# Performance work log

Measured on AMD Instinct MI355X. Metric: run time of the kernel, lower is better.

Reference implementation:

```python
import jax, jax.numpy as jnp
import numpy as np
import math

D_MODEL = 1024
NUM_HEADS = 16
DIM_FF = 4096
B, N = 4, 1024
GRID = 32
R_LEFT = 1.0
R_RIGHT = 1.0
LN_EPS = 1e-5


def get_alibi_slopes(n_heads):
    def pow2(n):
        start = 2 ** (-2 ** (-(math.log2(n) - 3)))
        return [start * start ** i for i in range(n)]
    if math.log2(n_heads).is_integer():
        slopes = pow2(n_heads)
    else:
        m = 2 ** math.floor(math.log2(n_heads))
        slopes = pow2(m)
        slopes += [slopes[-1] * 0.5 ** (i + 1) for i in range(n_heads - m)]
    return jnp.asarray(np.array(slopes, dtype=np.float32))


def setup_inputs() -> dict:
    key = jax.random.key(0)
    ks = jax.random.split(key, 16)
    s = 1.0 / math.sqrt(D_MODEL)
    inp = {
        "src": jax.random.normal(ks[0], (B, N, D_MODEL), jnp.float32),
        "coords": jax.random.randint(ks[1], (B, N, 2), 0, GRID, jnp.int32),
        "Wq": jax.random.normal(ks[2], (D_MODEL, D_MODEL), jnp.float32) * s,
        "Wk": jax.random.normal(ks[3], (D_MODEL, D_MODEL), jnp.float32) * s,
        "Wv": jax.random.normal(ks[4], (D_MODEL, D_MODEL), jnp.float32) * s,
        "Wo": jax.random.normal(ks[5], (D_MODEL, D_MODEL), jnp.float32) * s,
        "W1": jax.random.normal(ks[6], (DIM_FF, D_MODEL), jnp.float32) * s,
        "b1": jnp.zeros((DIM_FF,), jnp.float32),
        "W2": jax.random.normal(ks[7], (D_MODEL, DIM_FF), jnp.float32) * (1.0 / math.sqrt(DIM_FF)),
        "b2": jnp.zeros((D_MODEL,), jnp.float32),
        "g1": jnp.ones((D_MODEL,), jnp.float32),
        "be1": jnp.zeros((D_MODEL,), jnp.float32),
        "g2": jnp.ones((D_MODEL,), jnp.float32),
        "be2": jnp.zeros((D_MODEL,), jnp.float32),
    }
    return inp


def layer_norm(x, g, b):
    mu = jnp.mean(x, axis=-1, keepdims=True)
    var = jnp.mean(jnp.square(x - mu), axis=-1, keepdims=True)
    return (x - mu) * jax.lax.rsqrt(var + LN_EPS) * g + b


def alibi_2d_bias(coords, slopes):
    # coords: (B, N, 2) int -> bias (B, H, N, N)
    x = coords[..., 0].astype(jnp.float32)
    y = coords[..., 1].astype(jnp.float32)
    dist = jnp.abs(x[:, :, None] - x[:, None, :]) + jnp.abs(y[:, :, None] - y[:, None, :])
    flat = y * (x.max() + 1.0) + x  # global x.max(), matching torch code
    le = (flat[:, None, :] <= flat[:, :, None]).astype(jnp.float32)  # (B,N,N)
    s = slopes.reshape(1, -1, 1, 1)
    left = s * R_LEFT
    right = s * R_RIGHT
    return dist[:, None] * (le[:, None] * left + (1.0 - le[:, None]) * right)


def reference(src, coords, Wq, Wk, Wv, Wo, W1, b1, W2, b2, g1, be1, g2, be2):
    H, Hd = NUM_HEADS, D_MODEL // NUM_HEADS
    scale = Hd ** (-0.5)
    slopes = get_alibi_slopes(H)
    bias = alibi_2d_bias(coords, slopes)  # (B,H,N,N)

    Bn, Nn, D = src.shape
    q = (src @ Wq.T).reshape(Bn, Nn, H, Hd)
    k = (src @ Wk.T).reshape(Bn, Nn, H, Hd)
    v = (src @ Wv.T).reshape(Bn, Nn, H, Hd)
    attn = jnp.einsum("bnhd,bmhd->bhnm", q, k) * scale + bias
    attn = jax.nn.softmax(attn, axis=-1)
    out = jnp.einsum("bhnm,bmhd->bnhd", attn, v).reshape(Bn, Nn, D)
    src2 = out @ Wo.T

    x = layer_norm(src + src2, g1, be1)
    ff = (jax.nn.gelu(x @ W1.T + b1, approximate=False)) @ W2.T + b2
    return layer_norm(x + ff, g2, be2)
```

## Files before the change

### kernel.cpp

```cpp
#include <hip/hip_runtime.h>
#include <hip/hip_bf16.h>
#include <math.h>

#define DEV __device__ __forceinline__

typedef __attribute__((ext_vector_type(4))) float f32x4;
typedef __attribute__((ext_vector_type(16))) float f32x16;
typedef __attribute__((ext_vector_type(8))) short bf16x8;
typedef __attribute__((ext_vector_type(4))) unsigned short us4;

DEV unsigned short f2bf(float f) {
    union { float f; unsigned u; } v; v.f = f;
    unsigned r = v.u + 0x7FFF + ((v.u >> 16) & 1);
    return (unsigned short)(r >> 16);
}

DEV void async16(const void* g, void* l) {
    __builtin_amdgcn_global_load_lds(
        (const __attribute__((address_space(1))) void*)g,
        (__attribute__((address_space(3))) void*)l, 16, 0, 0);
}

DEV int xcd_swizzle(int flat, int nwg) {
    int q = nwg >> 3, r8 = nwg & 7;
    int xcd = flat & 7, idx = flat >> 3;
    return (xcd < r8 ? xcd * (q + 1) : r8 * (q + 1) + (xcd - r8) * q) + idx;
}

__global__ void cvt_kernel(const float* __restrict__ in, unsigned short* __restrict__ out, int n4) {
    int i = blockIdx.x * blockDim.x + threadIdx.x;
    if (i >= n4) return;
    f32x4 v = ((const f32x4*)in)[i];
    us4 o;
    o.x = f2bf(v.x); o.y = f2bf(v.y); o.z = f2bf(v.z); o.w = f2bf(v.w);
    ((us4*)out)[i] = o;
}

#define BM 128
#define BN 128
#define BKK 64

template<int EPI>
__global__ __launch_bounds__(256) void gemm_bt(
    const unsigned short* __restrict__ A,
    const unsigned short* __restrict__ B,
    float* __restrict__ Cf, unsigned short* __restrict__ Cb,
    const float* __restrict__ bias,
    int M, int N, int K)
{
    __shared__ unsigned short As[BM * BKK];
    __shared__ unsigned short Bs[BN * BKK];

    const int tid  = threadIdx.x;
    const int wid  = tid >> 6, lane = tid & 63;
    const int l15  = lane & 15, l16 = lane >> 4;
    const int wr   = wid >> 1, wc = wid & 1;

    const int nwg  = gridDim.x * gridDim.y;
    const int flat = xcd_swizzle(blockIdx.y * gridDim.x + blockIdx.x, nwg);
    const int row0 = (flat / gridDim.x) * BM;
    const int col0 = (flat % gridDim.x) * BN;

    f32x4 acc[4][4] = {};

    const int nkt = K / BKK;
    for (int kt = 0; kt < nkt; ++kt) {
        const int k0 = kt * BKK;
        __syncthreads();
#pragma unroll
        for (int i = 0; i < 4; ++i) {
            int c = i * 256 + tid;
            int row = c >> 3, slot = c & 7;
            int ks = (slot ^ (row & 7)) * 8;
            async16(A + (size_t)(row0 + row) * K + k0 + ks, (char*)As + c * 16);
            async16(B + (size_t)(col0 + row) * K + k0 + ks, (char*)Bs + c * 16);
        }
        __syncthreads();
#pragma unroll
        for (int kk = 0; kk < 2; ++kk) {
            bf16x8 af[4], bfr[4];
#pragma unroll
            for (int m = 0; m < 4; ++m) {
                int r = wr * 64 + m * 16 + l15;
                int slot = (kk * 4 + l16) ^ (r & 7);
                af[m] = *(const bf16x8*)((const char*)As + r * 128 + slot * 16);
            }
#pragma unroll
            for (int n = 0; n < 4; ++n) {
                int r = wc * 64 + n * 16 + l15;
                int slot = (kk * 4 + l16) ^ (r & 7);
                bfr[n] = *(const bf16x8*)((const char*)Bs + r * 128 + slot * 16);
            }
#pragma unroll
            for (int m = 0; m < 4; ++m)
#pragma unroll
                for (int n = 0; n < 4; ++n)
                    acc[m][n] = __builtin_amdgcn_mfma_f32_16x16x32_bf16(af[m], bfr[n], acc[m][n], 0, 0, 0);
        }
    }

#pragma unroll
    for (int m = 0; m < 4; ++m) {
        int grow = row0 + wr * 64 + m * 16 + l16 * 4;
#pragma unroll
        for (int n = 0; n < 4; ++n) {
            int gcol = col0 + wc * 64 + n * 16 + l15;
            float bv = (EPI >= 2) ? bias[gcol] : 0.f;
#pragma unroll
            for (int r = 0; r < 4; ++r) {
                float v = acc[m][n][r];
                size_t idx = (size_t)(grow + r) * N + gcol;
                if (EPI == 0) {
                    Cb[idx] = f2bf(v);
                } else if (EPI == 1) {
                    Cf[idx] = v;
                } else if (EPI == 2) {
                    v += bv;
                    v = 0.5f * v * (1.f + erff(v * 0.70710678118f));
                    Cb[idx] = f2bf(v);
                } else {
                    Cf[idx] = v + bv;
                }
            }
        }
    }
}

template<int EPI>
__global__ __launch_bounds__(512, 2) void gemm256(
    const unsigned short* __restrict__ A,
    const unsigned short* __restrict__ B,
    float* __restrict__ Cf, unsigned short* __restrict__ Cb,
    const float* __restrict__ bias,
    int M, int N, int K)
{
    __shared__ unsigned short As[2][256 * 64];
    __shared__ unsigned short Bs[2][256 * 64];

    const int tid = threadIdx.x;
    const int wid = tid >> 6, lane = tid & 63;
    const int l15 = lane & 15, l16 = lane >> 4;
    const int wr = wid >> 2, wc = wid & 3;

    const int nwg  = gridDim.x * gridDim.y;
    const int flat = xcd_swizzle(blockIdx.y * gridDim.x + blockIdx.x, nwg);
    const int row0 = (flat / gridDim.x) * 256;
    const int col0 = (flat % gridDim.x) * 256;

    f32x4 acc[8][4] = {};

    auto stage = [&](int buf, int k0) {
#pragma unroll
        for (int i = 0; i < 4; ++i) {
            int c = i * 512 + tid;
            int row = c >> 3, slot = c & 7;
            int ks = (slot ^ (row & 7)) * 8;
            async16(A + (size_t)(row0 + row) * K + k0 + ks, (char*)As[buf] + c * 16);
            async16(B + (size_t)(col0 + row) * K + k0 + ks, (char*)Bs[buf] + c * 16);
        }
    };

    stage(0, 0);
    int cur = 0;
    const int nkt = K / 64;
    for (int kt = 0; kt < nkt; ++kt) {
        __syncthreads();
        if (kt + 1 < nkt) stage(cur ^ 1, (kt + 1) * 64);
#pragma unroll
        for (int kk = 0; kk < 2; ++kk) {
            bf16x8 af[8], bfr[4];
#pragma unroll
            for (int m = 0; m < 8; ++m) {
                int r = wr * 128 + m * 16 + l15;
                int slot = (kk * 4 + l16) ^ (r & 7);
                af[m] = *(const bf16x8*)((const char*)As[cur] + r * 128 + slot * 16);
            }
#pragma unroll
            for (int n = 0; n < 4; ++n) {
                int r = wc * 64 + n * 16 + l15;
                int slot = (kk * 4 + l16) ^ (r & 7);
                bfr[n] = *(const bf16x8*)((const char*)Bs[cur] + r * 128 + slot * 16);
            }
            __builtin_amdgcn_s_setprio(1);
#pragma unroll
            for (int m = 0; m < 8; ++m)
#pragma unroll
                for (int n = 0; n < 4; ++n)
                    acc[m][n] = __builtin_amdgcn_mfma_f32_16x16x32_bf16(af[m], bfr[n], acc[m][n], 0, 0, 0);
            __builtin_amdgcn_s_setprio(0);
        }
        cur ^= 1;
    }

#pragma unroll
    for (int m = 0; m < 8; ++m) {
        int grow = row0 + wr * 128 + m * 16 + l16 * 4;
#pragma unroll
        for (int n = 0; n < 4; ++n) {
            int gcol = col0 + wc * 64 + n * 16 + l15;
            float bv = (EPI >= 2) ? bias[gcol] : 0.f;
#pragma unroll
            for (int r = 0; r < 4; ++r) {
                float v = acc[m][n][r];
                size_t idx = (size_t)(grow + r) * N + gcol;
                if (EPI == 0) {
                    Cb[idx] = f2bf(v);
                } else if (EPI == 1) {
                    Cf[idx] = v;
                } else if (EPI == 2) {
                    v += bv;
                    v = 0.5f * v * (1.f + erff(v * 0.70710678118f));
                    Cb[idx] = f2bf(v);
                } else {
                    Cf[idx] = v + bv;
                }
            }
        }
    }
}

__global__ __launch_bounds__(256) void transpose_v(const unsigned short* __restrict__ qkv,
                                                   unsigned short* __restrict__ vt)
{
    __shared__ unsigned short t[64][72];
    const int n0 = blockIdx.x * 64;
    const int bh = blockIdx.y;
    const int b = bh >> 4, h = bh & 15;
    const int tid = threadIdx.x;
#pragma unroll
    for (int i = 0; i < 2; ++i) {
        int c = i * 256 + tid;
        int row = c >> 3, col0 = (c & 7) * 8;
        const unsigned short* src = qkv + (size_t)(b * 1024 + n0 + row) * 3072 + 2048 + h * 64 + col0;
        bf16x8 v = *(const bf16x8*)src;
#pragma unroll
        for (int j = 0; j < 8; ++j) t[row][col0 + j] = (unsigned short)v[j];
    }
    __syncthreads();
#pragma unroll
    for (int i = 0; i < 2; ++i) {
        int c = i * 256 + tid;
        int hd = c >> 3, col0 = (c & 7) * 8;
        bf16x8 v;
#pragma unroll
        for (int j = 0; j < 8; ++j) v[j] = (short)t[col0 + j][hd];
        *(bf16x8*)(vt + ((size_t)bh * 64 + hd) * 1024 + n0 + col0) = v;
    }
}

__global__ __launch_bounds__(256) void attn_kernel(const unsigned short* __restrict__ qkv,
                                                   const int* __restrict__ coords,
                                                   const unsigned short* __restrict__ vt,
                                                   unsigned short* __restrict__ out)
{
    __shared__ unsigned short Ks[2][64 * 64];
    __shared__ unsigned short Vs[2][64 * 64];
    __shared__ float cF[1024 * 2];

    const int tid = threadIdx.x, wid = tid >> 6, lane = tid & 63;
    const int l31 = lane & 31, hi = lane >> 5;
    const int q0 = blockIdx.x * 128;
    const int bh = blockIdx.y;
    const int b = bh >> 4, h = bh & 15;
    const float LOG2E = 1.4426950408889634f;
    const float slope2 = exp2f(-0.5f * (float)(h + 1)) * LOG2E;
    const float scale2 = 0.125f * LOG2E;

    const int c0 = tid,       r0c = c0 >> 3, ks0 = ((c0 & 7) ^ (r0c & 7)) * 8;
    const int c1 = 256 + tid, r1c = c1 >> 3, ks1 = ((c1 & 7) ^ (r1c & 7)) * 8;
    const unsigned short* kbase = qkv + (size_t)(b * 1024) * 3072 + 1024 + h * 64;
    const unsigned short* vbase = vt + (size_t)bh * 64 * 1024;

    {
        const int2* cp = (const int2*)coords + b * 1024;
#pragma unroll
        for (int i = 0; i < 4; ++i) {
            int kv = i * 256 + tid;
            int2 c = cp[kv];
            cF[kv * 2]     = slope2 * (float)c.x;
            cF[kv * 2 + 1] = slope2 * (float)c.y;
        }
    }

    const int qrow = q0 + wid * 32 + l31;
    bf16x8 qf[4];
    {
        const unsigned short* qp = qkv + (size_t)(b * 1024 + qrow) * 3072 + h * 64 + hi * 8;
        qf[0] = *(const bf16x8*)qp;
        qf[1] = *(const bf16x8*)(qp + 16);
        qf[2] = *(const bf16x8*)(qp + 32);
        qf[3] = *(const bf16x8*)(qp + 48);
    }
    float qxs, qys;
    {
        int2 qc = ((const int2*)coords)[b * 1024 + qrow];
        qxs = slope2 * (float)qc.x; qys = slope2 * (float)qc.y;
    }

    float mr = -1e30f, lr = 0.f;
    f32x16 o0 = (f32x16)0.f, o1 = (f32x16)0.f;

    async16(kbase + (size_t)r0c * 3072 + ks0, (char*)Ks[0] + c0 * 16);
    async16(kbase + (size_t)r1c * 3072 + ks1, (char*)Ks[0] + c1 * 16);
    async16(vbase + (size_t)r0c * 1024 + ks0, (char*)Vs[0] + c0 * 16);
    async16(vbase + (size_t)r1c * 1024 + ks1, (char*)Vs[0] + c1 * 16);
    int cur = 0;

    for (int t = 0; t < 16; ++t) {
        const int kv0 = t * 64;
        __syncthreads();
        if (t < 15) {
            const int kv1 = kv0 + 64;
            async16(kbase + (size_t)(kv1 + r0c) * 3072 + ks0, (char*)Ks[cur ^ 1] + c0 * 16);
            async16(kbase + (size_t)(kv1 + r1c) * 3072 + ks1, (char*)Ks[cur ^ 1] + c1 * 16);
            async16(vbase + (size_t)r0c * 1024 + kv1 + ks0, (char*)Vs[cur ^ 1] + c0 * 16);
            async16(vbase + (size_t)r1c * 1024 + kv1 + ks1, (char*)Vs[cur ^ 1] + c1 * 16);
        }

        f32x16 s0 = (f32x16)0.f, s1 = (f32x16)0.f;
        __builtin_amdgcn_s_setprio(1);
#pragma unroll
        for (int c16 = 0; c16 < 4; ++c16) {
            int slot = ((c16 * 2 + hi) ^ (l31 & 7)) * 16;
            bf16x8 k0f = *(const bf16x8*)((const char*)Ks[cur] + l31 * 128 + slot);
            bf16x8 k1f = *(const bf16x8*)((const char*)Ks[cur] + (32 + l31) * 128 + slot);
            s0 = __builtin_amdgcn_mfma_f32_32x32x16_bf16(k0f, qf[c16], s0, 0, 0, 0);
            s1 = __builtin_amdgcn_mfma_f32_32x32x16_bf16(k1f, qf[c16], s1, 0, 0, 0);
        }
        __builtin_amdgcn_s_setprio(0);

#pragma unroll
        for (int T = 0; T < 2; ++T) {
            f32x16& S = T ? s1 : s0;
#pragma unroll
            for (int u = 0; u < 4; ++u) {
                int kvb = kv0 + T * 32 + u * 8 + hi * 4;
                f32x4 ca = *(const f32x4*)&cF[kvb * 2];
                f32x4 cb = *(const f32x4*)&cF[kvb * 2 + 4];
                S[4*u+0] = S[4*u+0] * scale2 + (fabsf(qxs - ca.x) + fabsf(qys - ca.y));
                S[4*u+1] = S[4*u+1] * scale2 + (fabsf(qxs - ca.z) + fabsf(qys - ca.w));
                S[4*u+2] = S[4*u+2] * scale2 + (fabsf(qxs - cb.x) + fabsf(qys - cb.y));
                S[4*u+3] = S[4*u+3] * scale2 + (fabsf(qxs - cb.z) + fabsf(qys - cb.w));
            }
        }

        float pm = s0[0];
#pragma unroll
        for (int i = 1; i < 16; ++i) pm = fmaxf(pm, s0[i]);
#pragma unroll
        for (int i = 0; i < 16; ++i) pm = fmaxf(pm, s1[i]);
        pm = fmaxf(pm, __shfl_xor(pm, 32, 64));
        if (__any(pm > mr + 8.0f)) {
            float mn = fmaxf(mr, pm);
            float corr = exp2f(mr - mn);
            mr = mn;
            lr *= corr;
#pragma unroll
            for (int i = 0; i < 16; ++i) { o0[i] *= corr; o1[i] *= corr; }
        }
        float sum = 0.f;
#pragma unroll
        for (int i = 0; i < 16; ++i) { float p = exp2f(s0[i] - mr); s0[i] = p; sum += p; }
#pragma unroll
        for (int i = 0; i < 16; ++i) { float p = exp2f(s1[i] - mr); s1[i] = p; sum += p; }
        sum += __shfl_xor(sum, 32, 64);
        lr += sum;

        bf16x8 pf[4];
#pragma unroll
        for (int c = 0; c < 4; ++c) {
            const f32x16& S = (c < 2) ? s0 : s1;
            const int e = (c & 1) * 8;
            unsigned x0, x1, y0, y1;
            asm("v_cvt_pk_bf16_f32 %0, %1, %2" : "=v"(x0) : "v"(S[e+0]), "v"(S[e+1]));
            asm("v_cvt_pk_bf16_f32 %0, %1, %2" : "=v"(x1) : "v"(S[e+2]), "v"(S[e+3]));
            asm("v_cvt_pk_bf16_f32 %0, %1, %2" : "=v"(y0) : "v"(S[e+4]), "v"(S[e+5]));
            asm("v_cvt_pk_bf16_f32 %0, %1, %2" : "=v"(y1) : "v"(S[e+6]), "v"(S[e+7]));
            asm("v_permlane32_swap_b32 %0, %1" : "+v"(x0), "+v"(y0));
            asm("v_permlane32_swap_b32 %0, %1" : "+v"(x1), "+v"(y1));
            union { unsigned u[4]; bf16x8 v; } pk_;
            pk_.u[0] = x0; pk_.u[1] = x1; pk_.u[2] = y0; pk_.u[3] = y1;
            pf[c] = pk_.v;
        }

        __builtin_amdgcn_s_setprio(1);
#pragma unroll
        for (int c = 0; c < 4; ++c) {
            int slot = ((c * 2 + hi) ^ (l31 & 7)) * 16;
            bf16x8 v0 = *(const bf16x8*)((const char*)Vs[cur] + l31 * 128 + slot);
            bf16x8 v1 = *(const bf16x8*)((const char*)Vs[cur] + (32 + l31) * 128 + slot);
            o0 = __builtin_amdgcn_mfma_f32_32x32x16_bf16(v0, pf[c], o0, 0, 0, 0);
            o1 = __builtin_amdgcn_mfma_f32_32x32x16_bf16(v1, pf[c], o1, 0, 0, 0);
        }
        __builtin_amdgcn_s_setprio(0);
        cur ^= 1;
    }

    const float inv = 1.0f / lr;
    unsigned short* op = out + (size_t)(b * 1024 + qrow) * 1024 + h * 64;
#pragma unroll
    for (int Td = 0; Td < 2; ++Td) {
        const f32x16& O = Td ? o1 : o0;
#pragma unroll
        for (int u = 0; u < 4; ++u) {
            us4 w;
            w.x = f2bf(O[4*u+0] * inv);
            w.y = f2bf(O[4*u+1] * inv);
            w.z = f2bf(O[4*u+2] * inv);
            w.w = f2bf(O[4*u+3] * inv);
            *(us4*)(op + Td * 32 + u * 8 + hi * 4) = w;
        }
    }
}

__global__ __launch_bounds__(256) void ln_kernel(const float* __restrict__ a, const float* __restrict__ bres,
                                                 const float* __restrict__ g, const float* __restrict__ be,
                                                 float* __restrict__ xout, unsigned short* __restrict__ xb)
{
    __shared__ float red[2][4];
    const int row = blockIdx.x, tid = threadIdx.x;
    const int wid = tid >> 6, lane = tid & 63;
    f32x4 v = ((const f32x4*)a)[(size_t)row * 256 + tid] + ((const f32x4*)bres)[(size_t)row * 256 + tid];
    float s1 = v.x + v.y + v.z + v.w;
    float s2 = v.x * v.x + v.y * v.y + v.z * v.z + v.w * v.w;
#pragma unroll
    for (int off = 1; off < 64; off <<= 1) {
        s1 += __shfl_xor(s1, off, 64);
        s2 += __shfl_xor(s2, off, 64);
    }
    if (lane == 0) { red[0][wid] = s1; red[1][wid] = s2; }
    __syncthreads();
    s1 = red[0][0] + red[0][1] + red[0][2] + red[0][3];
    s2 = red[1][0] + red[1][1] + red[1][2] + red[1][3];
    float mu = s1 * (1.f / 1024.f);
    float var = s2 * (1.f / 1024.f) - mu * mu;
    float rstd = rsqrtf(var + 1e-5f);
    f32x4 gv = ((const f32x4*)g)[tid], bev = ((const f32x4*)be)[tid];
    f32x4 y = (v - mu) * rstd * gv + bev;
    if (xout) ((f32x4*)xout)[(size_t)row * 256 + tid] = y;
    if (xb) {
        us4 ob;
        ob.x = f2bf(y.x); ob.y = f2bf(y.y); ob.z = f2bf(y.z); ob.w = f2bf(y.w);
        ((us4*)xb)[(size_t)row * 256 + tid] = ob;
    }
}

extern "C" void kernel_launch(void* const* d_in, const int* in_sizes, int n_in,
                              void* d_out, int out_size, void* d_ws, size_t ws_size,
                              hipStream_t stream) {
    const float* src    = (const float*)d_in[0];
    const int*   coords = (const int*)d_in[1];
    const float* Wq     = (const float*)d_in[2];
    const float* Wk     = (const float*)d_in[3];
    const float* Wv     = (const float*)d_in[4];
    const float* Wo     = (const float*)d_in[5];
    const float* W1     = (const float*)d_in[6];
    const float* b1     = (const float*)d_in[7];
    const float* W2     = (const float*)d_in[8];
    const float* b2     = (const float*)d_in[9];
    const float* g1     = (const float*)d_in[10];
    const float* be1    = (const float*)d_in[11];
    const float* g2     = (const float*)d_in[12];
    const float* be2    = (const float*)d_in[13];
    float* out = (float*)d_out;

    char* ws = (char*)d_ws;
    size_t off = 0;
    auto alloc = [&](size_t bytes) { size_t o = off; off += (bytes + 255) & ~(size_t)255; return o; };

    const size_t BT = 4096;
    size_t qkv_off   = alloc(BT * 3072 * 2);
    size_t attno_off = alloc(BT * 1024 * 2);
    size_t vt_off    = alloc((size_t)64 * 64 * 1024 * 2);
    size_t regionA_end = off;
    size_t x_off    = alloc(BT * 1024 * 4);
    size_t ffs_off  = alloc(BT * 1024 * 4);
    size_t srcb_off = alloc(BT * 1024 * 2);
    size_t wqkv_off = alloc((size_t)3072 * 1024 * 2);
    size_t wo_off   = alloc((size_t)1024 * 1024 * 2);
    size_t w1_off   = alloc((size_t)4096 * 1024 * 2);
    size_t w2_off   = alloc((size_t)1024 * 4096 * 2);
    (void)regionA_end; (void)ws_size; (void)in_sizes; (void)n_in; (void)out_size;

    unsigned short* qkv   = (unsigned short*)(ws + qkv_off);
    unsigned short* attno = (unsigned short*)(ws + attno_off);
    unsigned short* vt    = (unsigned short*)(ws + vt_off);
    float*          x     = (float*)(ws + x_off);
    float*          src2  = (float*)(ws + ffs_off);
    float*          ff    = (float*)(ws + ffs_off);
    unsigned short* srcb  = (unsigned short*)(ws + srcb_off);
    unsigned short* xb    = (unsigned short*)(ws + srcb_off);
    unsigned short* wqkvb = (unsigned short*)(ws + wqkv_off);
    unsigned short* wob   = (unsigned short*)(ws + wo_off);
    unsigned short* w1b   = (unsigned short*)(ws + w1_off);
    unsigned short* w2b   = (unsigned short*)(ws + w2_off);
    unsigned short* h1    = (unsigned short*)(ws + qkv_off);

    auto cvt = [&](const float* in, unsigned short* o, size_t n) {
        int n4 = (int)(n / 4);
        cvt_kernel<<<(n4 + 255) / 256, 256, 0, stream>>>(in, o, n4);
    };
    cvt(src, srcb, BT * 1024);
    cvt(Wq, wqkvb, 1024 * 1024);
    cvt(Wk, wqkvb + 1024 * 1024, 1024 * 1024);
    cvt(Wv, wqkvb + 2 * 1024 * 1024, 1024 * 1024);
    cvt(Wo, wob, 1024 * 1024);
    cvt(W1, w1b, 4096 * 1024);
    cvt(W2, w2b, 1024 * 4096);

    gemm_bt<0><<<dim3(3072 / BN, 4096 / BM), 256, 0, stream>>>(srcb, wqkvb, nullptr, qkv, nullptr, 4096, 3072, 1024);
    transpose_v<<<dim3(16, 64), 256, 0, stream>>>(qkv, vt);
    attn_kernel<<<dim3(8, 64), 256, 0, stream>>>(qkv, coords, vt, attno);
    gemm_bt<1><<<dim3(1024 / BN, 4096 / BM), 256, 0, stream>>>(attno, wob, src2, nullptr, nullptr, 4096, 1024, 1024);
    ln_kernel<<<4096, 256, 0, stream>>>(src, src2, g1, be1, x, xb);
    gemm256<2><<<dim3(4096 / 256, 4096 / 256), 512, 0, stream>>>(xb, w1b, nullptr, h1, b1, 4096, 4096, 1024);
    gemm_bt<3><<<dim3(1024 / BN, 4096 / BM), 256, 0, stream>>>(h1, w2b, ff, nullptr, b2, 4096, 1024, 4096);
    ln_kernel<<<4096, 256, 0, stream>>>(x, ff, g2, be2, out, nullptr);
}
```

Baseline: 400.2 us.

## Split-K the Wo and FF2 GEMMs with bf16 partials reduced in LayerNorm

```diff
diff --git a/kernel.cpp b/kernel.cpp
--- a/kernel.cpp
+++ b/kernel.cpp
@@ -13,6 +13,10 @@
     union { float f; unsigned u; } v; v.f = f;
     unsigned r = v.u + 0x7FFF + ((v.u >> 16) & 1);
     return (unsigned short)(r >> 16);
+}
+
+DEV float bf2f(unsigned short u) {
+    union { unsigned u; float f; } v; v.u = (unsigned)u << 16; return v.f;
 }
 
 DEV void async16(const void* g, void* l) {
@@ -126,6 +130,81 @@
     }
 }
 
+__global__ __launch_bounds__(256) void gemm_splitk(
+    const unsigned short* __restrict__ A,
+    const unsigned short* __restrict__ B,
+    unsigned short* __restrict__ Pb,
+    int N, int Kld, int Klen)
+{
+    __shared__ unsigned short As[BM * BKK];
+    __shared__ unsigned short Bs[BN * BKK];
+
+    const int tid  = threadIdx.x;
+    const int wid  = tid >> 6, lane = tid & 63;
+    const int l15  = lane & 15, l16 = lane >> 4;
+    const int wr   = wid >> 1, wc = wid & 1;
+
+    const int s = blockIdx.z;
+    const unsigned short* Ab = A + (size_t)s * Klen;
+    const unsigned short* Bb = B + (size_t)s * Klen;
+
+    const int nwg  = gridDim.x * gridDim.y;
+    const int flat = xcd_swizzle(blockIdx.y * gridDim.x + blockIdx.x, nwg);
+    const int row0 = (flat / gridDim.x) * BM;
+    const int col0 = (flat % gridDim.x) * BN;
+
+    f32x4 acc[4][4] = {};
+
+    const int nkt = Klen / BKK;
+    for (int kt = 0; kt < nkt; ++kt) {
+        const int k0 = kt * BKK;
+        __syncthreads();
+#pragma unroll
+        for (int i = 0; i < 4; ++i) {
+            int c = i * 256 + tid;
+            int row = c >> 3, slot = c & 7;
+            int ks = (slot ^ (row & 7)) * 8;
+            async16(Ab + (size_t)(row0 + row) * Kld + k0 + ks, (char*)As + c * 16);
+            async16(Bb + (size_t)(col0 + row) * Kld + k0 + ks, (char*)Bs + c * 16);
+        }
+        __syncthreads();
+#pragma unroll
+        for (int kk = 0; kk < 2; ++kk) {
+            bf16x8 af[4], bfr[4];
+#pragma unroll
+            for (int m = 0; m < 4; ++m) {
+                int r = wr * 64 + m * 16 + l15;
+                int slot = (kk * 4 + l16) ^ (r & 7);
+                af[m] = *(const bf16x8*)((const char*)As + r * 128 + slot * 16);
+            }
+#pragma unroll
+            for (int n = 0; n < 4; ++n) {
+                int r = wc * 64 + n * 16 + l15;
+                int slot = (kk * 4 + l16) ^ (r & 7);
+                bfr[n] = *(const bf16x8*)((const char*)Bs + r * 128 + slot * 16);
+            }
+#pragma unroll
+            for (int m = 0; m < 4; ++m)
+#pragma unroll
+                for (int n = 0; n < 4; ++n)
+                    acc[m][n] = __builtin_amdgcn_mfma_f32_16x16x32_bf16(af[m], bfr[n], acc[m][n], 0, 0, 0);
+        }
+    }
+
+    unsigned short* P = Pb + (size_t)s * (size_t)(gridDim.y * BM) * N;
+#pragma unroll
+    for (int m = 0; m < 4; ++m) {
+        int grow = row0 + wr * 64 + m * 16 + l16 * 4;
+#pragma unroll
+        for (int n = 0; n < 4; ++n) {
+            int gcol = col0 + wc * 64 + n * 16 + l15;
+#pragma unroll
+            for (int r = 0; r < 4; ++r)
+                P[(size_t)(grow + r) * N + gcol] = f2bf(acc[m][n][r]);
+        }
+    }
+}
+
 template<int EPI>
 __global__ __launch_bounds__(512, 2) void gemm256(
     const unsigned short* __restrict__ A,
@@ -413,14 +492,25 @@
     }
 }
 
-__global__ __launch_bounds__(256) void ln_kernel(const float* __restrict__ a, const float* __restrict__ bres,
-                                                 const float* __restrict__ g, const float* __restrict__ be,
-                                                 float* __restrict__ xout, unsigned short* __restrict__ xb)
+__global__ __launch_bounds__(256) void ln_sum_kernel(const float* __restrict__ a,
+                                                     const unsigned short* __restrict__ pb, int nsplit,
+                                                     const float* __restrict__ bias,
+                                                     const float* __restrict__ g, const float* __restrict__ be,
+                                                     float* __restrict__ xout, unsigned short* __restrict__ xb)
 {
     __shared__ float red[2][4];
     const int row = blockIdx.x, tid = threadIdx.x;
     const int wid = tid >> 6, lane = tid & 63;
-    f32x4 v = ((const f32x4*)a)[(size_t)row * 256 + tid] + ((const f32x4*)bres)[(size_t)row * 256 + tid];
+    const size_t idx = (size_t)row * 256 + tid;
+    f32x4 v = ((const f32x4*)a)[idx];
+    for (int s = 0; s < nsplit; ++s) {
+        us4 p = ((const us4*)pb)[(size_t)s * 1048576 + idx];
+        v.x += bf2f(p.x); v.y += bf2f(p.y); v.z += bf2f(p.z); v.w += bf2f(p.w);
+    }
+    if (bias) {
+        f32x4 bv = ((const f32x4*)bias)[tid];
+        v.x += bv.x; v.y += bv.y; v.z += bv.z; v.w += bv.w;
+    }
     float s1 = v.x + v.y + v.z + v.w;
     float s2 = v.x * v.x + v.y * v.y + v.z * v.z + v.w * v.w;
 #pragma unroll
@@ -437,11 +527,11 @@
     float rstd = rsqrtf(var + 1e-5f);
     f32x4 gv = ((const f32x4*)g)[tid], bev = ((const f32x4*)be)[tid];
     f32x4 y = (v - mu) * rstd * gv + bev;
-    if (xout) ((f32x4*)xout)[(size_t)row * 256 + tid] = y;
+    if (xout) ((f32x4*)xout)[idx] = y;
     if (xb) {
         us4 ob;
         ob.x = f2bf(y.x); ob.y = f2bf(y.y); ob.z = f2bf(y.z); ob.w = f2bf(y.w);
-        ((us4*)xb)[(size_t)row * 256 + tid] = ob;
+        ((us4*)xb)[idx] = ob;
     }
 }
 
@@ -472,7 +562,6 @@
     size_t qkv_off   = alloc(BT * 3072 * 2);
     size_t attno_off = alloc(BT * 1024 * 2);
     size_t vt_off    = alloc((size_t)64 * 64 * 1024 * 2);
-    size_t regionA_end = off;
     size_t x_off    = alloc(BT * 1024 * 4);
     size_t ffs_off  = alloc(BT * 1024 * 4);
     size_t srcb_off = alloc(BT * 1024 * 2);
@@ -480,14 +569,14 @@
     size_t wo_off   = alloc((size_t)1024 * 1024 * 2);
     size_t w1_off   = alloc((size_t)4096 * 1024 * 2);
     size_t w2_off   = alloc((size_t)1024 * 4096 * 2);
-    (void)regionA_end; (void)ws_size; (void)in_sizes; (void)n_in; (void)out_size;
+    (void)ws_size; (void)in_sizes; (void)n_in; (void)out_size;
 
     unsigned short* qkv   = (unsigned short*)(ws + qkv_off);
     unsigned short* attno = (unsigned short*)(ws + attno_off);
     unsigned short* vt    = (unsigned short*)(ws + vt_off);
     float*          x     = (float*)(ws + x_off);
-    float*          src2  = (float*)(ws + ffs_off);
-    float*          ff    = (float*)(ws + ffs_off);
+    unsigned short* pbWo  = (unsigned short*)(ws + ffs_off);
+    unsigned short* pbFF  = (unsigned short*)(ws + ffs_off);
     unsigned short* srcb  = (unsigned short*)(ws + srcb_off);
     unsigned short* xb    = (unsigned short*)(ws + srcb_off);
     unsigned short* wqkvb = (unsigned short*)(ws + wqkv_off);
@@ -511,9 +600,9 @@
     gemm_bt<0><<<dim3(3072 / BN, 4096 / BM), 256, 0, stream>>>(srcb, wqkvb, nullptr, qkv, nullptr, 4096, 3072, 1024);
     transpose_v<<<dim3(16, 64), 256, 0, stream>>>(qkv, vt);
     attn_kernel<<<dim3(8, 64), 256, 0, stream>>>(qkv, coords, vt, attno);
-    gemm_bt<1><<<dim3(1024 / BN, 4096 / BM), 256, 0, stream>>>(attno, wob, src2, nullptr, nullptr, 4096, 1024, 1024);
-    ln_kernel<<<4096, 256, 0, stream>>>(src, src2, g1, be1, x, xb);
+    gemm_splitk<<<dim3(1024 / BN, 4096 / BM, 2), 256, 0, stream>>>(attno, wob, pbWo, 1024, 1024, 512);
+    ln_sum_kernel<<<4096, 256, 0, stream>>>(src, pbWo, 2, nullptr, g1, be1, x, xb);
     gemm256<2><<<dim3(4096 / 256, 4096 / 256), 512, 0, stream>>>(xb, w1b, nullptr, h1, b1, 4096, 4096, 1024);
-    gemm_bt<3><<<dim3(1024 / BN, 4096 / BM), 256, 0, stream>>>(h1, w2b, ff, nullptr, b2, 4096, 1024, 4096);
-    ln_kernel<<<4096, 256, 0, stream>>>(x, ff, g2, be2, out, nullptr);
-}
+    gemm_splitk<<<dim3(1024 / BN, 4096 / BM, 4), 256, 0, stream>>>(h1, w2b, pbFF, 1024, 4096, 1024);
+    ln_sum_kernel<<<4096, 256, 0, stream>>>(x, pbFF, 4, b2, g2, be2, out, nullptr);
+}
```

Result: faster. 371.8 us (-7.1%).
